# Kernel optimization log

Measured on AMD Instinct MI355X. Metric: run time of the kernel, lower is better.

Reference implementation:

```python
import jax, jax.numpy as jnp
import numpy as np

B = 1024
INPUT_DIM = 768
NUM_CLASSES = 5
NUM_PRIMARY_CAPS = 32
PRIMARY_CAP_DIM = 8
ROUTING_CAP_DIM = 16
NUM_ITER = 3
PROJ_DIM = 256 * 6 * 6  # 9216
NUM_IN_CAPS = NUM_PRIMARY_CAPS * 16  # conv output is 4x4 spatial -> 512


def squash(t, axis=-1):
    sq = jnp.sum(t * t, axis=axis, keepdims=True)
    scale = sq / (1.0 + sq)
    return scale * t / jnp.sqrt(sq + 1e-8)


def setup_inputs() -> dict:
    key = jax.random.key(0)
    k = jax.random.split(key, 6)
    x = jax.random.normal(k[0], (B, INPUT_DIM), dtype=jnp.float32)
    W1 = jax.random.normal(k[1], (INPUT_DIM, PROJ_DIM), dtype=jnp.float32) * 0.02
    b1 = jnp.zeros((PROJ_DIM,), dtype=jnp.float32)
    convW = jax.random.normal(k[2], (NUM_PRIMARY_CAPS * PRIMARY_CAP_DIM, 256, 3, 3), dtype=jnp.float32) * 0.02  # OIHW
    convB = jnp.zeros((NUM_PRIMARY_CAPS * PRIMARY_CAP_DIM,), dtype=jnp.float32)
    # matches torch.randn init in RoutingCapsules: [num_in, num_out, out_dim, in_dim]
    Wr = jax.random.normal(k[3], (NUM_IN_CAPS, NUM_CLASSES, ROUTING_CAP_DIM, PRIMARY_CAP_DIM), dtype=jnp.float32)
    return {"x": x, "W1": W1, "b1": b1, "convW": convW, "convB": convB, "Wr": Wr}


def reference(x, W1, b1, convW, convB, Wr):
    # feature projection (dropout is identity in eval)
    h = jax.nn.relu(x @ W1 + b1)
    h = h.reshape(-1, 256, 6, 6)
    # primary capsules conv: k=3, s=1, pad=0 -> [B, 256, 4, 4]
    out = jax.lax.conv_general_dilated(h, convW, window_strides=(1, 1), padding='VALID',
                                       dimension_numbers=('NCHW', 'OIHW', 'NCHW'))
    out = out + convB[None, :, None, None]
    bsz = out.shape[0]
    out = out.reshape(bsz, NUM_PRIMARY_CAPS, PRIMARY_CAP_DIM, -1)      # [B,32,8,16]
    out = jnp.transpose(out, (0, 1, 3, 2)).reshape(bsz, -1, PRIMARY_CAP_DIM)  # [B,512,8]
    u = squash(out, axis=-1)
    # prediction vectors u_hat: [B, in_caps, out_caps, out_dim]
    u_hat = jnp.einsum('nodi,bni->bnod', Wr, u)
    # dynamic routing
    b_logits = jnp.zeros((bsz, NUM_IN_CAPS, NUM_CLASSES, 1), dtype=u_hat.dtype)
    v = None
    for it in range(NUM_ITER):
        c = jax.nn.softmax(b_logits, axis=2)
        s = jnp.sum(c * u_hat, axis=1)  # [B, out_caps, out_dim]
        v = squash(s, axis=-1)
        if it < NUM_ITER - 1:
            agreement = jnp.sum(u_hat * v[:, None], axis=-1, keepdims=True)
            b_logits = b_logits + agreement
    class_probs = jnp.sqrt(jnp.sum(v * v, axis=-1))
    return (class_probs, v)
```

## Files before the change

kernel.cpp:

```cpp
#include <hip/hip_runtime.h>
#include <hip/hip_fp16.h>

#define BSZ   1024
#define INDIM 768
#define PROJ  9216
#define NCAP  512
#define NCLS  5
#define K2    2304

typedef __bf16    bf16x8 __attribute__((ext_vector_type(8)));
typedef _Float16  f16x8  __attribute__((ext_vector_type(8)));
typedef float     f32x4  __attribute__((ext_vector_type(4)));
typedef _Float16  h2     __attribute__((ext_vector_type(2)));

static __device__ __forceinline__ unsigned short f2bf(float f) {
  unsigned int x = __float_as_uint(f);
  return (unsigned short)((x + 0x7fffu + ((x >> 16) & 1u)) >> 16);
}
static __device__ __forceinline__ float bf2f(unsigned int u) {
  return __uint_as_float(u << 16);
}

#if defined(__has_builtin)
#if __has_builtin(__builtin_amdgcn_fdot2)
#define HAVE_FDOT2 1
#endif
#endif
static __device__ __forceinline__ float fdot2(h2 a, h2 b, float c) {
#ifdef HAVE_FDOT2
  return __builtin_amdgcn_fdot2(a, b, c, false);
#else
  return c + (float)a[0] * (float)b[0] + (float)a[1] * (float)b[1];
#endif
}
static __device__ __forceinline__ h2 u2h2(unsigned int u) {
  return __builtin_bit_cast(h2, u);
}
static __device__ __forceinline__ unsigned short f2h(float f) {
  return __builtin_bit_cast(unsigned short, (_Float16)f);
}

static __device__ __forceinline__ void gload16(const void* g, void* l) {
  auto gp = reinterpret_cast<const unsigned int __attribute__((address_space(1)))*>(
      (unsigned long long)g);
  auto lp = reinterpret_cast<unsigned int __attribute__((address_space(3)))*>(
      (unsigned long long)l);
  __builtin_amdgcn_global_load_lds(gp, lp, 16, 0, 0);
}

template <int RELU, int OBF16>
__global__ __launch_bounds__(256) void mfma_gemm(
    const unsigned short* __restrict__ A,
    const unsigned short* __restrict__ Bt,
    const float* __restrict__ bias,
    void* __restrict__ Cout,
    int M, int N, int K) {
  __shared__ __align__(16) unsigned short smem[16384];
  const int t    = threadIdx.x;
  const int bn   = blockIdx.x * 128;
  const int bm   = blockIdx.y * 128;
  const int lane = t & 63;
  const int wid  = t >> 6;
  const int wm   = (wid >> 1) * 64;
  const int wn   = (wid & 1) * 64;
  const int l15  = lane & 15;
  const int kb   = lane >> 4;

  const int r0 = t >> 2,         kc = t & 3;
  const int r1 = (t + 256) >> 2;
  const int gk0 = ((kc ^ (r0 & 3)) << 3);
  const int gk1 = ((kc ^ (r1 & 3)) << 3);

  const unsigned short* Ar0 = A  + (size_t)(bm + r0) * K + gk0;
  const unsigned short* Ar1 = A  + (size_t)(bm + r1) * K + gk1;
  const unsigned short* Br0 = Bt + (size_t)(bn + r0) * K + gk0;
  const unsigned short* Br1 = Bt + (size_t)(bn + r1) * K + gk1;

  int aoff[4], boff[4];
#pragma unroll
  for (int i = 0; i < 4; ++i) {
    const int ra = wm + i * 16 + l15;
    aoff[i] = ra * 32 + ((kb ^ (ra & 3)) << 3);
    const int rb = wn + i * 16 + l15;
    boff[i] = 4096 + rb * 32 + ((kb ^ (rb & 3)) << 3);
  }

  f32x4 acc[4][4];
#pragma unroll
  for (int i = 0; i < 4; ++i)
#pragma unroll
    for (int j = 0; j < 4; ++j)
#pragma unroll
      for (int q = 0; q < 4; ++q) acc[i][j][q] = 0.f;

  const int nk = K >> 5;
  gload16(Ar0, &smem[t * 8]);
  gload16(Ar1, &smem[(t + 256) * 8]);
  gload16(Br0, &smem[4096 + t * 8]);
  gload16(Br1, &smem[4096 + (t + 256) * 8]);
  __syncthreads();

  int buf = 0;
  for (int ks = 0; ks < nk; ++ks) {
    if (ks + 1 < nk) {
      const int k = (ks + 1) << 5;
      const int o = (buf ^ 1) * 8192;
      gload16(Ar0 + k, &smem[o + t * 8]);
      gload16(Ar1 + k, &smem[o + (t + 256) * 8]);
      gload16(Br0 + k, &smem[o + 4096 + t * 8]);
      gload16(Br1 + k, &smem[o + 4096 + (t + 256) * 8]);
    }
    const unsigned short* base = &smem[buf * 8192];
    bf16x8 af[4], bfr[4];
#pragma unroll
    for (int i = 0; i < 4; ++i) {
      af[i]  = *(const bf16x8*)(base + aoff[i]);
      bfr[i] = *(const bf16x8*)(base + boff[i]);
    }
#pragma unroll
    for (int i = 0; i < 4; ++i)
#pragma unroll
      for (int j = 0; j < 4; ++j)
        acc[i][j] = __builtin_amdgcn_mfma_f32_16x16x32_bf16(af[i], bfr[j], acc[i][j], 0, 0, 0);
    __syncthreads();
    buf ^= 1;
  }

#pragma unroll
  for (int j = 0; j < 4; ++j) {
    const int col = bn + wn + j * 16 + l15;
    const float bv = bias[col];
#pragma unroll
    for (int i = 0; i < 4; ++i) {
#pragma unroll
      for (int q = 0; q < 4; ++q) {
        const int row = bm + wm + i * 16 + kb * 4 + q;
        float v = acc[i][j][q] + bv;
        if (RELU) v = fmaxf(v, 0.f);
        if (OBF16) ((unsigned short*)Cout)[(size_t)row * N + col] = f2bf(v);
        else       ((float*)Cout)[(size_t)row * N + col] = v;
      }
    }
  }
}

__global__ __launch_bounds__(256) void conv_gemm(
    const unsigned short* __restrict__ ht,
    const unsigned short* __restrict__ Wt2,
    const float* __restrict__ convB,
    unsigned short* __restrict__ cv) {
  __shared__ __align__(16) unsigned short smem[12288];
  const int t    = threadIdx.x;
  const int bn   = blockIdx.x * 128;
  const int bm   = blockIdx.y * 64;
  const int lane = t & 63, wid = t >> 6;
  const int l15  = lane & 15, kb = lane >> 4;

  const int ar  = t >> 2, asg = t & 3;
  const int ab  = (bm + ar) >> 4, ap = (bm + ar) & 15;
  const int spb = (ap >> 2) * 6 + (ap & 3);
  const unsigned short* abase =
      ht + (size_t)ab * PROJ + spb * 256 + ((asg ^ (ar & 3)) << 3);

  const int br0 = t >> 2, br1 = (t + 256) >> 2, bsg = t & 3;
  const unsigned short* bb0 = Wt2 + (size_t)(bn + br0) * K2 + ((bsg ^ (br0 & 3)) << 3);
  const unsigned short* bb1 = Wt2 + (size_t)(bn + br1) * K2 + ((bsg ^ (br1 & 3)) << 3);

  int aoff[4], boff[2];
#pragma unroll
  for (int i = 0; i < 4; ++i) {
    const int ra = i * 16 + l15;
    aoff[i] = ra * 32 + ((kb ^ (ra & 3)) << 3);
  }
#pragma unroll
  for (int j = 0; j < 2; ++j) {
    const int rb = wid * 32 + j * 16 + l15;
    boff[j] = 2048 + rb * 32 + ((kb ^ (rb & 3)) << 3);
  }

  f32x4 acc[4][2];
#pragma unroll
  for (int i = 0; i < 4; ++i)
#pragma unroll
    for (int j = 0; j < 2; ++j)
#pragma unroll
      for (int q = 0; q < 4; ++q) acc[i][j][q] = 0.f;

  auto stage = [&](int ks, int buf) {
    const int tap = ks >> 3;
    const int dsp = tap + 3 * (tap / 3);
    const int ic0 = (ks & 7) << 5;
    unsigned short* sb = &smem[buf * 6144];
    gload16(abase + dsp * 256 + ic0, sb + t * 8);
    gload16(bb0 + ks * 32, sb + 2048 + t * 8);
    gload16(bb1 + ks * 32, sb + 2048 + (t + 256) * 8);
  };

  stage(0, 0);
  __syncthreads();

  int buf = 0;
  for (int ks = 0; ks < 72; ++ks) {
    if (ks + 1 < 72) stage(ks + 1, buf ^ 1);
    const unsigned short* base = &smem[buf * 6144];
    bf16x8 af[4], bfr[2];
#pragma unroll
    for (int i = 0; i < 4; ++i) af[i] = *(const bf16x8*)(base + aoff[i]);
#pragma unroll
    for (int j = 0; j < 2; ++j) bfr[j] = *(const bf16x8*)(base + boff[j]);
#pragma unroll
    for (int i = 0; i < 4; ++i)
#pragma unroll
      for (int j = 0; j < 2; ++j)
        acc[i][j] = __builtin_amdgcn_mfma_f32_16x16x32_bf16(af[i], bfr[j], acc[i][j], 0, 0, 0);
    __syncthreads();
    buf ^= 1;
  }

#pragma unroll
  for (int j = 0; j < 2; ++j) {
    const int col = bn + wid * 32 + j * 16 + l15;
    const float bv = convB[col];
#pragma unroll
    for (int i = 0; i < 4; ++i)
#pragma unroll
      for (int q = 0; q < 4; ++q) {
        const int row = bm + i * 16 + kb * 4 + q;
        cv[(size_t)row * 256 + col] = f2h(acc[i][j][q] + bv);
      }
  }
}

__global__ __launch_bounds__(256) void convert_bf16(const float* __restrict__ in,
                                                    unsigned short* __restrict__ out,
                                                    int n4) {
  const int i = blockIdx.x * 256 + threadIdx.x;
  if (i >= n4) return;
  float4 v = ((const float4*)in)[i];
  ushort4 o;
  o.x = f2bf(v.x); o.y = f2bf(v.y); o.z = f2bf(v.z); o.w = f2bf(v.w);
  ((ushort4*)out)[i] = o;
}

__global__ __launch_bounds__(256) void convert_f16(const float* __restrict__ in,
                                                   __half2* __restrict__ out, int n4) {
  const int i = blockIdx.x * 256 + threadIdx.x;
  if (i >= n4) return;
  float4 v = ((const float4*)in)[i];
  out[i * 2]     = __floats2half2_rn(v.x, v.y);
  out[i * 2 + 1] = __floats2half2_rn(v.z, v.w);
}

__global__ __launch_bounds__(256) void transpose_w1_perm(const float* __restrict__ W,
                                                         unsigned short* __restrict__ Wt) {
  __shared__ float tile[32][33];
  const int n0 = blockIdx.x * 32, k0 = blockIdx.y * 32;
  const int r = threadIdx.x >> 3, c = (threadIdx.x & 7) * 4;
  float4 v = *(const float4*)(W + (size_t)(k0 + r) * PROJ + n0 + c);
  tile[r][c] = v.x; tile[r][c + 1] = v.y; tile[r][c + 2] = v.z; tile[r][c + 3] = v.w;
  __syncthreads();
  ushort4 o;
  o.x = f2bf(tile[c + 0][r]); o.y = f2bf(tile[c + 1][r]);
  o.z = f2bf(tile[c + 2][r]); o.w = f2bf(tile[c + 3][r]);
  const int nn = n0 + r;
  const int prow = (nn % 36) * 256 + nn / 36;
  *(ushort4*)(Wt + (size_t)prow * INDIM + k0 + c) = o;
}

__global__ __launch_bounds__(256) void perm_bias(const float* __restrict__ b1,
                                                 float* __restrict__ pb1) {
  const int n = blockIdx.x * 256 + threadIdx.x;
  if (n >= PROJ) return;
  pb1[(n % 36) * 256 + n / 36] = b1[n];
}

__global__ __launch_bounds__(256) void convw_prep2(const float* __restrict__ W,
                                                   unsigned short* __restrict__ Wt2) {
  const int id = blockIdx.x * 256 + threadIdx.x;
  const int oc = id >> 8, ic = id & 255;
  const float* s = W + (size_t)id * 9;
#pragma unroll
  for (int tap = 0; tap < 9; ++tap)
    Wt2[(size_t)oc * K2 + tap * 256 + ic] = f2bf(s[tap]);
}

__global__ __launch_bounds__(256) void squash_u(const unsigned short* __restrict__ cv,
                                                __half2* __restrict__ U) {
  const int b = blockIdx.x;
  const int t = threadIdx.x;
#pragma unroll
  for (int h = 0; h < 2; ++h) {
    const int id = t + h * 256;
    const int cap = id & 31, p = id >> 5;
    const unsigned short* s = cv + ((size_t)b * 16 + p) * 256 + cap * 8;
    uint4 qv = *(const uint4*)s;
    h2 a0 = u2h2(qv.x), a1 = u2h2(qv.y), a2 = u2h2(qv.z), a3 = u2h2(qv.w);
    float f0 = a0[0], f1 = a0[1], f2 = a1[0], f3 = a1[1];
    float f4 = a2[0], f5 = a2[1], f6 = a3[0], f7 = a3[1];
    float sq = f0 * f0 + f1 * f1 + f2 * f2 + f3 * f3 +
               f4 * f4 + f5 * f5 + f6 * f6 + f7 * f7;
    const float scale = sq / (1.f + sq) / sqrtf(sq + 1e-8f);
    __half2* d = U + ((size_t)b * 4096 + cap * 128 + p * 8) / 2;
    d[0] = __floats2half2_rn(f0 * scale, f1 * scale);
    d[1] = __floats2half2_rn(f2 * scale, f3 * scale);
    d[2] = __floats2half2_rn(f4 * scale, f5 * scale);
    d[3] = __floats2half2_rn(f6 * scale, f7 * scale);
  }
}

__global__ __launch_bounds__(512) void uhat_gemm(
    const unsigned short* __restrict__ U,
    const unsigned short* __restrict__ Wrh,
    unsigned short* __restrict__ uhat,
    float* __restrict__ s0q,
    int b0, int CB) {
  __shared__ float sred[8][16][80];
  const int mt = blockIdx.x, q = blockIdx.y;
  const int t = threadIdx.x, wid = t >> 6, lane = t & 63;
  const int l15 = lane & 15, kb = lane >> 4;
  const int bm = mt * 16;
  const int gb = b0 + bm;

  f32x4 sacc[5];
#pragma unroll
  for (int j = 0; j < 5; ++j)
#pragma unroll
    for (int r = 0; r < 4; ++r) sacc[j][r] = 0.f;

  const uint4 zz = make_uint4(0, 0, 0, 0);
#pragma unroll
  for (int i = 0; i < 8; ++i) {
    const int n = q * 64 + wid * 8 + i;
    uint4 av = zz;
    if (kb == 0) av = *(const uint4*)(U + (size_t)(gb + l15) * 4096 + n * 8);
    const f16x8 uf = __builtin_bit_cast(f16x8, av);
#pragma unroll
    for (int jn = 0; jn < 5; ++jn) {
      uint4 wv = zz;
      if (kb == 0) wv = *(const uint4*)(Wrh + (size_t)n * 640 + (jn * 16 + l15) * 8);
      f32x4 z;
      z[0] = 0.f; z[1] = 0.f; z[2] = 0.f; z[3] = 0.f;
      f32x4 c = __builtin_amdgcn_mfma_f32_16x16x32_f16(
          __builtin_bit_cast(f16x8, wv), uf, z, 0, 0, 0);
      ushort4 st;
      st.x = f2h(c[0]); st.y = f2h(c[1]); st.z = f2h(c[2]); st.w = f2h(c[3]);
      *(ushort4*)(uhat + ((size_t)(bm + l15) * 512 + n) * 80 + jn * 16 + kb * 4) = st;
#pragma unroll
      for (int qq = 0; qq < 4; ++qq) sacc[jn][qq] += c[qq];
    }
  }

#pragma unroll
  for (int jn = 0; jn < 5; ++jn)
#pragma unroll
    for (int qq = 0; qq < 4; ++qq)
      sred[wid][l15][jn * 16 + kb * 4 + qq] = sacc[jn][qq];
  __syncthreads();
#pragma unroll
  for (int k = 0; k < 3; ++k) {
    const int id = t + k * 512;
    if (id < 1280) {
      const int bb = id / 80, od = id % 80;
      float val = 0.f;
#pragma unroll
      for (int w = 0; w < 8; ++w) val += sred[w][bb][od];
      s0q[((size_t)q * CB + bm + bb) * 80 + od] = val;
    }
  }
}

template <int MODE>
__global__ __launch_bounds__(256) void route_pass(
    const unsigned short* __restrict__ uhat,
    const float* __restrict__ s0q,
    const float* __restrict__ vsum_in,
    float* __restrict__ vsum_out,
    float* __restrict__ out,
    int b0, int CB) {
  __shared__ unsigned int vph2[40];
  __shared__ float red[4][2][40];
  const int bl = blockIdx.x;
  const int b  = b0 + bl;
  const int t  = threadIdx.x;

  float v0r = 0.f;
  if (t < 80) {
    if (MODE == 1) {
      float s = 0.f;
#pragma unroll
      for (int g = 0; g < 8; ++g) s += s0q[((size_t)g * CB + bl) * 80 + t];
      s *= 0.2f;
      float sq = s * s;
      sq += __shfl_xor(sq, 1);
      sq += __shfl_xor(sq, 2);
      sq += __shfl_xor(sq, 4);
      sq += __shfl_xor(sq, 8);
      const float scale = sq / (1.f + sq) / sqrtf(sq + 1e-8f);
      v0r = s * scale;
    } else {
      v0r = vsum_in[(size_t)bl * 80 + t];
    }
    const float vnext = __shfl_down(v0r, 1);
    if ((t & 1) == 0)
      vph2[t >> 1] = __builtin_bit_cast(unsigned int, __floats2half2_rn(v0r, vnext));
  }
  __syncthreads();

  const int p = t >> 1, h = t & 1;
  float acc[5][8];
#pragma unroll
  for (int o = 0; o < 5; ++o)
#pragma unroll
    for (int j = 0; j < 8; ++j) acc[o][j] = 0.f;

  const unsigned short* ub = uhat + (size_t)bl * 40960;
  for (int c4 = 0; c4 < 4; ++c4) {
    const int n = c4 * 128 + p;
    const unsigned short* row = ub + n * 80 + h * 8;
    uint4 uv[5];
#pragma unroll
    for (int o = 0; o < 5; ++o) uv[o] = *(const uint4*)(row + o * 16);
    float ap[5];
#pragma unroll
    for (int o = 0; o < 5; ++o) {
      const int vb = o * 8 + h * 4;
      float a = fdot2(u2h2(uv[o].x), u2h2(vph2[vb]), 0.f);
      a = fdot2(u2h2(uv[o].y), u2h2(vph2[vb + 1]), a);
      a = fdot2(u2h2(uv[o].z), u2h2(vph2[vb + 2]), a);
      a = fdot2(u2h2(uv[o].w), u2h2(vph2[vb + 3]), a);
      ap[o] = a + __shfl_xor(a, 1);
    }
    float m = ap[0];
#pragma unroll
    for (int o = 1; o < 5; ++o) m = fmaxf(m, ap[o]);
    float es = 0.f, e[5];
#pragma unroll
    for (int o = 0; o < 5; ++o) { e[o] = __expf(ap[o] - m); es += e[o]; }
    const float inv = 1.f / es;
#pragma unroll
    for (int o = 0; o < 5; ++o) {
      const float cc = e[o] * inv;
      h2 hx = u2h2(uv[o].x), hy = u2h2(uv[o].y), hz = u2h2(uv[o].z), hw = u2h2(uv[o].w);
      acc[o][0] += cc * (float)hx[0]; acc[o][1] += cc * (float)hx[1];
      acc[o][2] += cc * (float)hy[0]; acc[o][3] += cc * (float)hy[1];
      acc[o][4] += cc * (float)hz[0]; acc[o][5] += cc * (float)hz[1];
      acc[o][6] += cc * (float)hw[0]; acc[o][7] += cc * (float)hw[1];
    }
  }

#pragma unroll
  for (int off = 2; off <= 32; off <<= 1)
#pragma unroll
    for (int o = 0; o < 5; ++o)
#pragma unroll
      for (int j = 0; j < 8; ++j) acc[o][j] += __shfl_xor(acc[o][j], off);
  const int wid = t >> 6, lane = t & 63;
  if (lane < 2) {
#pragma unroll
    for (int o = 0; o < 5; ++o)
#pragma unroll
      for (int j = 0; j < 8; ++j) red[wid][lane][o * 8 + j] = acc[o][j];
  }
  __syncthreads();

  if (t < 80) {
    const int o = t >> 4, d = t & 15, hh = d >> 3, dl = d & 7;
    const int c = o * 8 + dl;
    float s = red[0][hh][c] + red[1][hh][c] + red[2][hh][c] + red[3][hh][c];
    float sq = s * s;
    sq += __shfl_xor(sq, 1);
    sq += __shfl_xor(sq, 2);
    sq += __shfl_xor(sq, 4);
    sq += __shfl_xor(sq, 8);
    const float scale = sq / (1.f + sq) / sqrtf(sq + 1e-8f);
    const float vn = s * scale;
    if (MODE == 1) {
      vsum_out[(size_t)bl * 80 + t] = v0r + vn;
    } else {
      out[5 * BSZ + (size_t)b * 80 + t] = vn;
      float vv = vn * vn;
      vv += __shfl_xor(vv, 1);
      vv += __shfl_xor(vv, 2);
      vv += __shfl_xor(vv, 4);
      vv += __shfl_xor(vv, 8);
      if ((t & 15) == 0) out[(size_t)b * 5 + o] = sqrtf(vv);
    }
  }
}

extern "C" void kernel_launch(void* const* d_in, const int* in_sizes, int n_in,
                              void* d_out, int out_size, void* d_ws, size_t ws_size,
                              hipStream_t stream) {
  const float* x     = (const float*)d_in[0];
  const float* W1    = (const float*)d_in[1];
  const float* b1    = (const float*)d_in[2];
  const float* convW = (const float*)d_in[3];
  const float* convB = (const float*)d_in[4];
  const float* Wr    = (const float*)d_in[5];
  float* out = (float*)d_out;

  char* base = (char*)d_ws;
  size_t off = 0;
  auto alloc = [&](size_t bytes) { size_t o = off; off = (off + bytes + 255) & ~(size_t)255; return o; };
  const size_t o_wrh  = alloc((size_t)NCAP * 640 * 2);
  const size_t o_u    = alloc((size_t)BSZ * 4096 * 2);
  const size_t o_s0q  = alloc((size_t)8 * BSZ * 80 * 4);
  const size_t o_vsum = alloc((size_t)BSZ * 80 * 4);
  const size_t o_pool = off;
  size_t poff = o_pool;
  auto palloc = [&](size_t bytes) { size_t o = poff; poff = (poff + bytes + 255) & ~(size_t)255; return o; };
  const size_t o_ht  = palloc((size_t)BSZ * PROJ * 2);
  const size_t o_w1t = palloc((size_t)PROJ * INDIM * 2);
  const size_t o_xb  = palloc((size_t)BSZ * INDIM * 2);
  const size_t o_wt2 = palloc((size_t)256 * K2 * 2);
  const size_t o_pb1 = palloc((size_t)PROJ * 4);
  const size_t o_cv  = palloc((size_t)BSZ * 16 * 256 * 2);

  unsigned short* ht   = (unsigned short*)(base + o_ht);
  unsigned short* w1t  = (unsigned short*)(base + o_w1t);
  unsigned short* xb   = (unsigned short*)(base + o_xb);
  unsigned short* wt2  = (unsigned short*)(base + o_wt2);
  float*          pb1  = (float*)(base + o_pb1);
  unsigned short* wrh  = (unsigned short*)(base + o_wrh);
  unsigned short* cv   = (unsigned short*)(base + o_cv);
  __half2*        u    = (__half2*)(base + o_u);
  float*          s0q  = (float*)(base + o_s0q);
  float*          vsum = (float*)(base + o_vsum);
  unsigned short* uhat = (unsigned short*)(base + o_pool);

  convert_bf16<<<(BSZ * INDIM / 4 + 255) / 256, 256, 0, stream>>>(x, xb, BSZ * INDIM / 4);
  transpose_w1_perm<<<dim3(PROJ / 32, INDIM / 32), 256, 0, stream>>>(W1, w1t);
  perm_bias<<<PROJ / 256, 256, 0, stream>>>(b1, pb1);
  convw_prep2<<<256, 256, 0, stream>>>(convW, wt2);
  convert_f16<<<(NCAP * 640 / 4 + 255) / 256, 256, 0, stream>>>(Wr, (__half2*)wrh, NCAP * 640 / 4);

  mfma_gemm<1, 1><<<dim3(PROJ / 128, BSZ / 128), 256, 0, stream>>>(
      xb, w1t, pb1, (void*)ht, BSZ, PROJ, INDIM);

  conv_gemm<<<dim3(2, 256), 256, 0, stream>>>(ht, wt2, convB, cv);

  squash_u<<<BSZ, 256, 0, stream>>>(cv, u);

  const size_t pool_sz = ws_size > o_pool ? ws_size - o_pool : 0;
  int CB = 1024;
  while (CB > 16 && (size_t)CB * 512 * 80 * 2 > pool_sz) CB >>= 1;
  for (int b0 = 0; b0 < BSZ; b0 += CB) {
    uhat_gemm<<<dim3(CB / 16, 8), 512, 0, stream>>>(
        (const unsigned short*)u, wrh, uhat, s0q, b0, CB);
    route_pass<1><<<CB, 256, 0, stream>>>(uhat, s0q, nullptr, vsum, out, b0, CB);
    route_pass<2><<<CB, 256, 0, stream>>>(uhat, nullptr, vsum, nullptr, out, b0, CB);
  }
}
```

Before: 160.3 us.

## Fuse squash into conv GEMM epilogue and double the K-step tile

The separate squash kernel and its fp16 intermediate buffer are removed. The capsule squash is now computed in the conv GEMM epilogue, using lane shuffles across the 8 output channels of each capsule, and written straight into the U layout. The conv GEMM K-step also grows from 32 to 64 per stage (36 iterations instead of 72), with an 8-segment XOR swizzle and twice the LDS. This cuts one launch and an intermediate round trip through global memory, but the epilogue now does scattered 2-byte stores and the kernel uses more shared memory.

```diff
diff --git a/kernel.cpp b/kernel.cpp
--- a/kernel.cpp
+++ b/kernel.cpp
@@ -144,39 +144,50 @@
   }
 }
 
-__global__ __launch_bounds__(256) void conv_gemm(
+__global__ __launch_bounds__(256) void conv_gemm_sq(
     const unsigned short* __restrict__ ht,
     const unsigned short* __restrict__ Wt2,
     const float* __restrict__ convB,
-    unsigned short* __restrict__ cv) {
-  __shared__ __align__(16) unsigned short smem[12288];
+    unsigned short* __restrict__ U) {
+  __shared__ __align__(16) unsigned short smem[24576];
   const int t    = threadIdx.x;
   const int bn   = blockIdx.x * 128;
   const int bm   = blockIdx.y * 64;
   const int lane = t & 63, wid = t >> 6;
   const int l15  = lane & 15, kb = lane >> 4;
 
-  const int ar  = t >> 2, asg = t & 3;
-  const int ab  = (bm + ar) >> 4, ap = (bm + ar) & 15;
-  const int spb = (ap >> 2) * 6 + (ap & 3);
-  const unsigned short* abase =
-      ht + (size_t)ab * PROJ + spb * 256 + ((asg ^ (ar & 3)) << 3);
-
-  const int br0 = t >> 2, br1 = (t + 256) >> 2, bsg = t & 3;
-  const unsigned short* bb0 = Wt2 + (size_t)(bn + br0) * K2 + ((bsg ^ (br0 & 3)) << 3);
-  const unsigned short* bb1 = Wt2 + (size_t)(bn + br1) * K2 + ((bsg ^ (br1 & 3)) << 3);
-
-  int aoff[4], boff[2];
-#pragma unroll
-  for (int i = 0; i < 4; ++i) {
-    const int ra = i * 16 + l15;
-    aoff[i] = ra * 32 + ((kb ^ (ra & 3)) << 3);
-  }
-#pragma unroll
-  for (int j = 0; j < 2; ++j) {
-    const int rb = wid * 32 + j * 16 + l15;
-    boff[j] = 2048 + rb * 32 + ((kb ^ (rb & 3)) << 3);
-  }
+  const unsigned short* asrc[2];
+#pragma unroll
+  for (int cc = 0; cc < 2; ++cc) {
+    const int c = t + cc * 256;
+    const int row = c >> 3, seg = c & 7;
+    const int gr = bm + row, b = gr >> 4, p = gr & 15;
+    const int spb = (p >> 2) * 6 + (p & 3);
+    asrc[cc] = ht + (size_t)b * PROJ + spb * 256 + ((seg ^ (row & 7)) << 3);
+  }
+  const unsigned short* bsrc[4];
+#pragma unroll
+  for (int cc = 0; cc < 4; ++cc) {
+    const int c = t + cc * 256;
+    const int row = c >> 3, seg = c & 7;
+    bsrc[cc] = Wt2 + (size_t)(bn + row) * K2 + ((seg ^ (row & 7)) << 3);
+  }
+
+  int aoff[4][2], boff[2][2];
+#pragma unroll
+  for (int i = 0; i < 4; ++i)
+#pragma unroll
+    for (int kk = 0; kk < 2; ++kk) {
+      const int row = i * 16 + l15, seg = kk * 4 + kb;
+      aoff[i][kk] = row * 64 + ((seg ^ (row & 7)) << 3);
+    }
+#pragma unroll
+  for (int j = 0; j < 2; ++j)
+#pragma unroll
+    for (int kk = 0; kk < 2; ++kk) {
+      const int row = wid * 32 + j * 16 + l15, seg = kk * 4 + kb;
+      boff[j][kk] = 4096 + row * 64 + ((seg ^ (row & 7)) << 3);
+    }
 
   f32x4 acc[4][2];
 #pragma unroll
@@ -187,47 +198,65 @@
       for (int q = 0; q < 4; ++q) acc[i][j][q] = 0.f;
 
   auto stage = [&](int ks, int buf) {
-    const int tap = ks >> 3;
-    const int dsp = tap + 3 * (tap / 3);
-    const int ic0 = (ks & 7) << 5;
-    unsigned short* sb = &smem[buf * 6144];
-    gload16(abase + dsp * 256 + ic0, sb + t * 8);
-    gload16(bb0 + ks * 32, sb + 2048 + t * 8);
-    gload16(bb1 + ks * 32, sb + 2048 + (t + 256) * 8);
+    const int tap  = ks >> 2;
+    const int aofs = (tap + 3 * (tap / 3)) * 256 + ((ks & 3) << 6);
+    const int bofs = ks << 6;
+    unsigned short* sb = &smem[buf * 12288];
+    gload16(asrc[0] + aofs, sb + t * 8);
+    gload16(asrc[1] + aofs, sb + t * 8 + 2048);
+    gload16(bsrc[0] + bofs, sb + 4096 + t * 8);
+    gload16(bsrc[1] + bofs, sb + 4096 + t * 8 + 2048);
+    gload16(bsrc[2] + bofs, sb + 4096 + t * 8 + 4096);
+    gload16(bsrc[3] + bofs, sb + 4096 + t * 8 + 6144);
   };
 
   stage(0, 0);
   __syncthreads();
 
   int buf = 0;
-  for (int ks = 0; ks < 72; ++ks) {
-    if (ks + 1 < 72) stage(ks + 1, buf ^ 1);
-    const unsigned short* base = &smem[buf * 6144];
-    bf16x8 af[4], bfr[2];
-#pragma unroll
-    for (int i = 0; i < 4; ++i) af[i] = *(const bf16x8*)(base + aoff[i]);
-#pragma unroll
-    for (int j = 0; j < 2; ++j) bfr[j] = *(const bf16x8*)(base + boff[j]);
+  for (int ks = 0; ks < 36; ++ks) {
+    if (ks + 1 < 36) stage(ks + 1, buf ^ 1);
+    const unsigned short* base = &smem[buf * 12288];
+    bf16x8 af[4][2], bfr[2][2];
 #pragma unroll
     for (int i = 0; i < 4; ++i)
 #pragma unroll
-      for (int j = 0; j < 2; ++j)
-        acc[i][j] = __builtin_amdgcn_mfma_f32_16x16x32_bf16(af[i], bfr[j], acc[i][j], 0, 0, 0);
+      for (int kk = 0; kk < 2; ++kk) af[i][kk] = *(const bf16x8*)(base + aoff[i][kk]);
+#pragma unroll
+    for (int j = 0; j < 2; ++j)
+#pragma unroll
+      for (int kk = 0; kk < 2; ++kk) bfr[j][kk] = *(const bf16x8*)(base + boff[j][kk]);
+#pragma unroll
+    for (int kk = 0; kk < 2; ++kk)
+#pragma unroll
+      for (int i = 0; i < 4; ++i)
+#pragma unroll
+        for (int j = 0; j < 2; ++j)
+          acc[i][j] = __builtin_amdgcn_mfma_f32_16x16x32_bf16(af[i][kk], bfr[j][kk], acc[i][j], 0, 0, 0);
     __syncthreads();
     buf ^= 1;
   }
 
 #pragma unroll
   for (int j = 0; j < 2; ++j) {
-    const int col = bn + wid * 32 + j * 16 + l15;
-    const float bv = convB[col];
-#pragma unroll
-    for (int i = 0; i < 4; ++i)
+    const int oc  = bn + wid * 32 + j * 16 + l15;
+    const int cap = oc >> 3, ii = oc & 7;
+    const float bv = convB[oc];
+#pragma unroll
+    for (int i = 0; i < 4; ++i) {
 #pragma unroll
       for (int q = 0; q < 4; ++q) {
         const int row = bm + i * 16 + kb * 4 + q;
-        cv[(size_t)row * 256 + col] = f2h(acc[i][j][q] + bv);
+        const int b = row >> 4, p = row & 15;
+        const float val = acc[i][j][q] + bv;
+        float sq = val * val;
+        sq += __shfl_xor(sq, 1);
+        sq += __shfl_xor(sq, 2);
+        sq += __shfl_xor(sq, 4);
+        const float scale = sq / (1.f + sq) / sqrtf(sq + 1e-8f);
+        U[(size_t)b * 4096 + cap * 128 + p * 8 + ii] = f2h(val * scale);
       }
+    }
   }
 }
 
@@ -282,30 +311,6 @@
 #pragma unroll
   for (int tap = 0; tap < 9; ++tap)
     Wt2[(size_t)oc * K2 + tap * 256 + ic] = f2bf(s[tap]);
-}
-
-__global__ __launch_bounds__(256) void squash_u(const unsigned short* __restrict__ cv,
-                                                __half2* __restrict__ U) {
-  const int b = blockIdx.x;
-  const int t = threadIdx.x;
-#pragma unroll
-  for (int h = 0; h < 2; ++h) {
-    const int id = t + h * 256;
-    const int cap = id & 31, p = id >> 5;
-    const unsigned short* s = cv + ((size_t)b * 16 + p) * 256 + cap * 8;
-    uint4 qv = *(const uint4*)s;
-    h2 a0 = u2h2(qv.x), a1 = u2h2(qv.y), a2 = u2h2(qv.z), a3 = u2h2(qv.w);
-    float f0 = a0[0], f1 = a0[1], f2 = a1[0], f3 = a1[1];
-    float f4 = a2[0], f5 = a2[1], f6 = a3[0], f7 = a3[1];
-    float sq = f0 * f0 + f1 * f1 + f2 * f2 + f3 * f3 +
-               f4 * f4 + f5 * f5 + f6 * f6 + f7 * f7;
-    const float scale = sq / (1.f + sq) / sqrtf(sq + 1e-8f);
-    __half2* d = U + ((size_t)b * 4096 + cap * 128 + p * 8) / 2;
-    d[0] = __floats2half2_rn(f0 * scale, f1 * scale);
-    d[1] = __floats2half2_rn(f2 * scale, f3 * scale);
-    d[2] = __floats2half2_rn(f4 * scale, f5 * scale);
-    d[3] = __floats2half2_rn(f6 * scale, f7 * scale);
-  }
 }
 
 __global__ __launch_bounds__(512) void uhat_gemm(
@@ -514,7 +519,6 @@
   const size_t o_xb  = palloc((size_t)BSZ * INDIM * 2);
   const size_t o_wt2 = palloc((size_t)256 * K2 * 2);
   const size_t o_pb1 = palloc((size_t)PROJ * 4);
-  const size_t o_cv  = palloc((size_t)BSZ * 16 * 256 * 2);
 
   unsigned short* ht   = (unsigned short*)(base + o_ht);
   unsigned short* w1t  = (unsigned short*)(base + o_w1t);
@@ -522,8 +526,7 @@
   unsigned short* wt2  = (unsigned short*)(base + o_wt2);
   float*          pb1  = (float*)(base + o_pb1);
   unsigned short* wrh  = (unsigned short*)(base + o_wrh);
-  unsigned short* cv   = (unsigned short*)(base + o_cv);
-  __half2*        u    = (__half2*)(base + o_u);
+  unsigned short* u    = (unsigned short*)(base + o_u);
   float*          s0q  = (float*)(base + o_s0q);
   float*          vsum = (float*)(base + o_vsum);
   unsigned short* uhat = (unsigned short*)(base + o_pool);
@@ -537,16 +540,14 @@
   mfma_gemm<1, 1><<<dim3(PROJ / 128, BSZ / 128), 256, 0, stream>>>(
       xb, w1t, pb1, (void*)ht, BSZ, PROJ, INDIM);
 
-  conv_gemm<<<dim3(2, 256), 256, 0, stream>>>(ht, wt2, convB, cv);
-
-  squash_u<<<BSZ, 256, 0, stream>>>(cv, u);
+  conv_gemm_sq<<<dim3(2, 256), 256, 0, stream>>>(ht, wt2, convB, u);
 
   const size_t pool_sz = ws_size > o_pool ? ws_size - o_pool : 0;
   int CB = 1024;
   while (CB > 16 && (size_t)CB * 512 * 80 * 2 > pool_sz) CB >>= 1;
   for (int b0 = 0; b0 < BSZ; b0 += CB) {
     uhat_gemm<<<dim3(CB / 16, 8), 512, 0, stream>>>(
-        (const unsigned short*)u, wrh, uhat, s0q, b0, CB);
+        u, wrh, uhat, s0q, b0, CB);
     route_pass<1><<<CB, 256, 0, stream>>>(uhat, s0q, nullptr, vsum, out, b0, CB);
     route_pass<2><<<CB, 256, 0, stream>>>(uhat, nullptr, vsum, nullptr, out, b0, CB);
   }
```

Measured after the change: 152.8 us. 1.05x faster.
